# Kernel tuning notes

Hardware: AMD Instinct MI355X
Metric: run time of the kernel (lower is better)

The kernel has to match this reference:

```python
import jax, jax.numpy as jnp
import numpy as np

RADIUS = 1.0
NSAMPLE = 32


def _query_ball(new_xyz, xyz, radius, nsample):
    # new_xyz (B,M,3), xyz (B,N,3) -> idx (B,M,nsample) int32
    B, M, _ = new_xyz.shape
    N = xyz.shape[1]
    # squared distances via ||q||^2 + ||p||^2 - 2 q.p (avoids BxMxNx3 diff tensor)
    q2 = jnp.sum(new_xyz * new_xyz, axis=-1)          # (B,M)
    p2 = jnp.sum(xyz * xyz, axis=-1)                  # (B,N)
    qp = jnp.einsum('bmd,bnd->bmn', new_xyz, xyz)     # (B,M,N)
    dist2 = q2[:, :, None] + p2[:, None, :] - 2.0 * qp
    mask = dist2 < radius * radius
    ar = jnp.arange(N, dtype=jnp.int32)
    masked = jnp.where(mask, ar[None, None, :], jnp.int32(N + 1))  # (B,M,N)
    first = jnp.sort(masked, axis=2)[:, :, :nsample]               # (B,M,S)
    first_valid = first[:, :, :1]                                   # pad with first neighbor
    idx = jnp.where(first == N + 1, first_valid, first)
    return idx.astype(jnp.int32)


def _group(points, idx):
    # points (B,C,N), idx (B,M,S) -> (B,C,M,S) gather along N
    B, C, N = points.shape
    M, S = idx.shape[1], idx.shape[2]
    ie = jnp.broadcast_to(idx.reshape(B, 1, M * S).astype(jnp.int32), (B, C, M * S))
    return jnp.take_along_axis(points, ie, axis=2).reshape(B, C, M, S)


def setup_inputs() -> dict:
    key = jax.random.key(0)
    k1, k2 = jax.random.split(key)
    B, N, M, C = 8, 8192, 2048, 64
    xyz = jax.random.normal(k1, (B, N, 3), dtype=jnp.float32)
    # centroids are a subset of the cloud -> every ball query has >= 1 valid neighbor
    new_xyz = xyz[:, :M, :]
    features = jax.random.normal(k2, (B, C, N), dtype=jnp.float32)
    return {"xyz": xyz, "new_xyz": new_xyz, "features": features}


def reference(xyz, new_xyz, features):
    idx = _query_ball(new_xyz, xyz, RADIUS, NSAMPLE)                      # (B,M,S)
    grouped_xyz = _group(jnp.swapaxes(xyz, 1, 2), idx)                    # (B,3,M,S)
    grouped_xyz = grouped_xyz - jnp.swapaxes(new_xyz, 1, 2)[..., None]    # recenter
    grouped_feat = _group(features, idx)                                  # (B,C,M,S)
    return jnp.concatenate([grouped_xyz, grouped_feat], axis=1)           # (B,3+C,M,S)
```

## Files before the change

### kernel.cpp

```cpp
#include <hip/hip_runtime.h>

#define N_PTS 8192
#define M_Q   2048
#define C_F   64
#define NS    32
#define B_SZ  8

__global__ __launch_bounds__(256) void prep_kernel(
    const float* __restrict__ feat, const float* __restrict__ xyz,
    float* __restrict__ featT, float4* __restrict__ xyz4)
{
#pragma clang fp contract(off)
    __shared__ float lds[C_F * 65];
    if (blockIdx.x < B_SZ * 128) {
        const int b  = blockIdx.x >> 7;
        const int n0 = (blockIdx.x & 127) * 64;
        {
            const int c4 = threadIdx.x >> 6;
            const int nn = threadIdx.x & 63;
#pragma unroll
            for (int k = 0; k < 16; ++k) {
                const int c = k * 4 + c4;
                lds[c * 65 + nn] = feat[((size_t)b * C_F + c) * N_PTS + n0 + nn];
            }
        }
        __syncthreads();
        {
            const int n4 = threadIdx.x >> 6;
            const int c  = threadIdx.x & 63;
#pragma unroll
            for (int k = 0; k < 16; ++k) {
                const int nn = k * 4 + n4;
                featT[((size_t)b * N_PTS + n0 + nn) * C_F + c] = lds[c * 65 + nn];
            }
        }
    } else {
        const int i = (blockIdx.x - B_SZ * 128) * 256 + (int)threadIdx.x;
        const float p0 = xyz[i * 3 + 0];
        const float p1 = xyz[i * 3 + 1];
        const float p2 = xyz[i * 3 + 2];
        const float s  = (p0 * p0 + p1 * p1) + p2 * p2;
        xyz4[i] = make_float4(p0, p1, p2, s);
    }
}

__global__ __launch_bounds__(256) void qbg_kernel(
    const float4* __restrict__ xyz4, const float* __restrict__ nxyz,
    const float* __restrict__ featT, float* __restrict__ out)
{
#pragma clang fp contract(off)
    __shared__ int sidx[4][NS];

    const int lane = threadIdx.x & 63;
    const int w    = threadIdx.x >> 6;
    const int q    = blockIdx.x * 4 + w;
    const int b    = q >> 11;
    const float4* __restrict__ xb = xyz4 + (size_t)b * N_PTS;

    {
        const float* __restrict__ qp = nxyz + (size_t)q * 3;
        const float qx = qp[0], qy = qp[1], qz = qp[2];
        const float q2 = (qx * qx + qy * qy) + qz * qz;

        int  cnt = 0;
        int  first_idx = 0;
        bool have_first = false;

        float4 P[4], Pn[4];
#pragma unroll
        for (int cc = 0; cc < 4; ++cc) P[cc] = xb[cc * 64 + lane];

        for (int base = 0; base < N_PTS && cnt < NS; base += 256) {
            const int nb = base + 256;
            if (nb < N_PTS) {
#pragma unroll
                for (int cc = 0; cc < 4; ++cc) Pn[cc] = xb[nb + cc * 64 + lane];
            }
#pragma unroll
            for (int cc = 0; cc < 4; ++cc) {
                if (cnt >= NS) break;
                const float qpdot = (qx * P[cc].x + qy * P[cc].y) + qz * P[cc].z;
                const float d2 = (q2 + P[cc].w) - 2.0f * qpdot;
                const bool pred = d2 < 1.0f;
                const unsigned long long mask = __ballot(pred);
                if (mask) {
                    if (!have_first) {
                        first_idx = base + cc * 64 + __ffsll(mask) - 1;
                        have_first = true;
                    }
                    if (pred) {
                        const int pos = cnt + (int)__popcll(mask & ((1ull << lane) - 1ull));
                        if (pos < NS) sidx[w][pos] = base + cc * 64 + lane;
                    }
                    cnt += (int)__popcll(mask);
                }
            }
#pragma unroll
            for (int cc = 0; cc < 4; ++cc) P[cc] = Pn[cc];
        }
        if (cnt < NS) {
            for (int p = cnt + lane; p < NS; p += 64) sidx[w][p] = first_idx;
        }
    }
    __syncthreads();

    const int j  = threadIdx.x & 3;
    const int s  = (threadIdx.x >> 2) & 31;
    const int qs = threadIdx.x >> 7;
    const size_t cstride = (size_t)M_Q * NS;

    for (int g = 0; g < 2; ++g) {
        const int widx = g * 2 + qs;
        const int qq   = blockIdx.x * 4 + widx;
        const int mm   = qq & (M_Q - 1);
        const int n    = sidx[widx][s];

        const float* __restrict__ fb =
            featT + ((size_t)b * N_PTS + n) * C_F + j * 16;
        const float4 v0 = ((const float4*)fb)[0];
        const float4 v1 = ((const float4*)fb)[1];
        const float4 v2 = ((const float4*)fb)[2];
        const float4 v3 = ((const float4*)fb)[3];
        const float f[16] = { v0.x, v0.y, v0.z, v0.w,  v1.x, v1.y, v1.z, v1.w,
                              v2.x, v2.y, v2.z, v2.w,  v3.x, v3.y, v3.z, v3.w };

        const size_t obase = ((size_t)b * 67 * M_Q + mm) * NS + s;
        float* __restrict__ op = out + obase + (size_t)(3 + j * 16) * cstride;
#pragma unroll
        for (int i = 0; i < 16; ++i)
            op[(size_t)i * cstride] = f[i];

        if (j == 0) {
            const float4 pv = xb[n];
            const float* __restrict__ qp2 = nxyz + (size_t)qq * 3;
            float* __restrict__ ox = out + obase;
            ox[0]           = pv.x - qp2[0];
            ox[cstride]     = pv.y - qp2[1];
            ox[2 * cstride] = pv.z - qp2[2];
        }
    }
}

extern "C" void kernel_launch(void* const* d_in, const int* in_sizes, int n_in,
                              void* d_out, int out_size, void* d_ws, size_t ws_size,
                              hipStream_t stream)
{
    const float* xyz  = (const float*)d_in[0];
    const float* nxyz = (const float*)d_in[1];
    const float* feat = (const float*)d_in[2];
    float* out = (float*)d_out;

    float*  featT = (float*)d_ws;
    float4* xyz4  = (float4*)((char*)d_ws + (20 << 20));

    const int Q = B_SZ * M_Q;

    prep_kernel<<<B_SZ * 128 + (B_SZ * N_PTS) / 256, 256, 0, stream>>>(
        feat, xyz, featT, xyz4);
    qbg_kernel<<<Q / 4, 256, 0, stream>>>(xyz4, nxyz, featT, out);
}
```

Before: 187.4 us.

## Remap gather threads to emit float4 output stores and drop software prefetch

The gather phase is remapped so each thread handles 4 consecutive samples and one float4 channel group. It loads four neighbor feature vectors and transposes them in registers, so every output write becomes a 16-byte vector store instead of scalar strided stores. The recentered xyz output is written the same way, by three lanes per sample group. The double-buffered prefetch of point coordinates in the ball-query loop is also removed, which lowers register use but exposes load latency.

After: 184.3 us. About the same (-1.6%).

```diff
diff --git a/kernel.cpp b/kernel.cpp
--- a/kernel.cpp
+++ b/kernel.cpp
@@ -66,16 +66,11 @@
         int  first_idx = 0;
         bool have_first = false;
 
-        float4 P[4], Pn[4];
+        for (int base = 0; base < N_PTS && cnt < NS; base += 256) {
+            float4 P[4];
 #pragma unroll
-        for (int cc = 0; cc < 4; ++cc) P[cc] = xb[cc * 64 + lane];
-
-        for (int base = 0; base < N_PTS && cnt < NS; base += 256) {
-            const int nb = base + 256;
-            if (nb < N_PTS) {
-#pragma unroll
-                for (int cc = 0; cc < 4; ++cc) Pn[cc] = xb[nb + cc * 64 + lane];
-            }
+            for (int cc = 0; cc < 4; ++cc)
+                P[cc] = xb[base + cc * 64 + lane];
 #pragma unroll
             for (int cc = 0; cc < 4; ++cc) {
                 if (cnt >= NS) break;
@@ -95,8 +90,6 @@
                     cnt += (int)__popcll(mask);
                 }
             }
-#pragma unroll
-            for (int cc = 0; cc < 4; ++cc) P[cc] = Pn[cc];
         }
         if (cnt < NS) {
             for (int p = cnt + lane; p < NS; p += 64) sidx[w][p] = first_idx;
@@ -104,39 +97,46 @@
     }
     __syncthreads();
 
-    const int j  = threadIdx.x & 3;
-    const int s  = (threadIdx.x >> 2) & 31;
-    const int qs = threadIdx.x >> 7;
+    const int half = threadIdx.x >> 7;
+    const int hid  = threadIdx.x & 127;
+    const int c4   = hid & 15;
+    const int s4   = hid >> 4;
     const size_t cstride = (size_t)M_Q * NS;
 
+    const float4* __restrict__ fT =
+        (const float4*)(featT + (size_t)b * N_PTS * C_F);
+
     for (int g = 0; g < 2; ++g) {
-        const int widx = g * 2 + qs;
+        const int widx = g * 2 + half;
         const int qq   = blockIdx.x * 4 + widx;
         const int mm   = qq & (M_Q - 1);
-        const int n    = sidx[widx][s];
 
-        const float* __restrict__ fb =
-            featT + ((size_t)b * N_PTS + n) * C_F + j * 16;
-        const float4 v0 = ((const float4*)fb)[0];
-        const float4 v1 = ((const float4*)fb)[1];
-        const float4 v2 = ((const float4*)fb)[2];
-        const float4 v3 = ((const float4*)fb)[3];
-        const float f[16] = { v0.x, v0.y, v0.z, v0.w,  v1.x, v1.y, v1.z, v1.w,
-                              v2.x, v2.y, v2.z, v2.w,  v3.x, v3.y, v3.z, v3.w };
+        const int n0 = sidx[widx][s4 * 4 + 0];
+        const int n1 = sidx[widx][s4 * 4 + 1];
+        const int n2 = sidx[widx][s4 * 4 + 2];
+        const int n3 = sidx[widx][s4 * 4 + 3];
 
-        const size_t obase = ((size_t)b * 67 * M_Q + mm) * NS + s;
-        float* __restrict__ op = out + obase + (size_t)(3 + j * 16) * cstride;
-#pragma unroll
-        for (int i = 0; i < 16; ++i)
-            op[(size_t)i * cstride] = f[i];
+        const float4 L0 = fT[(size_t)n0 * 16 + c4];
+        const float4 L1 = fT[(size_t)n1 * 16 + c4];
+        const float4 L2 = fT[(size_t)n2 * 16 + c4];
+        const float4 L3 = fT[(size_t)n3 * 16 + c4];
 
-        if (j == 0) {
-            const float4 pv = xb[n];
-            const float* __restrict__ qp2 = nxyz + (size_t)qq * 3;
-            float* __restrict__ ox = out + obase;
-            ox[0]           = pv.x - qp2[0];
-            ox[cstride]     = pv.y - qp2[1];
-            ox[2 * cstride] = pv.z - qp2[2];
+        const size_t obase = ((size_t)b * 67 * M_Q + mm) * NS + s4 * 4;
+        float* __restrict__ op = out + obase + (size_t)(3 + c4 * 4) * cstride;
+        *(float4*)(op + 0 * cstride) = make_float4(L0.x, L1.x, L2.x, L3.x);
+        *(float4*)(op + 1 * cstride) = make_float4(L0.y, L1.y, L2.y, L3.y);
+        *(float4*)(op + 2 * cstride) = make_float4(L0.z, L1.z, L2.z, L3.z);
+        *(float4*)(op + 3 * cstride) = make_float4(L0.w, L1.w, L2.w, L3.w);
+
+        if (c4 < 3) {
+            const float qc = nxyz[qq * 3 + c4];
+            const float* __restrict__ xf = (const float*)xb;
+            float4 v;
+            v.x = xf[n0 * 4 + c4] - qc;
+            v.y = xf[n1 * 4 + c4] - qc;
+            v.z = xf[n2 * 4 + c4] - qc;
+            v.w = xf[n3 * 4 + c4] - qc;
+            *(float4*)(out + obase + (size_t)c4 * cstride) = v;
         }
     }
 }
```
